# Kernel tuning notes

Measured on AMD Instinct MI355X. Metric: run time of the kernel, lower is better.

The kernel has to match this reference:

```python
import jax, jax.numpy as jnp
import numpy as np

HIDDEN_DIM = 4096
NUM_SHARDS = 64
TOP_K = 2
B = 16384


def setup_inputs() -> dict:
    key = jax.random.key(0)
    k_h, k_w = jax.random.split(key)
    h = jax.random.normal(k_h, (B, HIDDEN_DIM), dtype=jnp.float32)
    # nn.init.normal_(weight, std=0.02); bias zeros
    weight = jax.random.normal(k_w, (NUM_SHARDS, HIDDEN_DIM), dtype=jnp.float32) * 0.02
    bias = jnp.zeros((NUM_SHARDS,), dtype=jnp.float32)
    return {"h": h, "weight": weight, "bias": bias}


def reference(h, weight, bias):
    # logits: (B, num_shards)
    logits = jnp.einsum("bd,ed->be", h, weight) + bias
    probs = jax.nn.softmax(logits, axis=-1)
    k = min(TOP_K, weight.shape[0])
    topk_vals, topk_idx = jax.lax.top_k(probs, k)
    denom = jnp.maximum(jnp.sum(topk_vals, axis=-1, keepdims=True), 1e-12)
    topk_w = topk_vals / denom
    return topk_w, topk_idx
```

## Files before the change

kernel.cpp:

```cpp
#include <hip/hip_runtime.h>
#include <hip/hip_bf16.h>
#include <math.h>


#define HIDDEN 4096
#define NSHARD 64
#define B_ROWS 16384

typedef short bf16x8 __attribute__((ext_vector_type(8)));
typedef float f32x4  __attribute__((ext_vector_type(4)));

__device__ __forceinline__ unsigned short f32_to_bf16_rn(float f) {
    __hip_bfloat16 h = __float2bfloat16(f);
    return *reinterpret_cast<unsigned short*>(&h);
}
__device__ __forceinline__ float bf16_bits_to_f32(unsigned short u) {
    union { unsigned int i; float f; } v; v.i = ((unsigned int)u) << 16;
    return v.f;
}

__device__ __forceinline__ void bf16_split(float f, short* hi, short* lo) {
    const unsigned int u = __float_as_uint(f);
    const unsigned int r = u + 0x7fffu + ((u >> 16) & 1u);
    *hi = (short)(r >> 16);
    union { unsigned int i; float f2; } hv; hv.i = r & 0xffff0000u;
    const float res = f - hv.f2;
    const unsigned int u2 = __float_as_uint(res);
    *lo = (short)((u2 + 0x7fffu + ((u2 >> 16) & 1u)) >> 16);
}

__global__ __launch_bounds__(256)
void wsplit_kernel(const float* __restrict__ w,
                   unsigned short* __restrict__ w_hi,
                   unsigned short* __restrict__ w_lo)
{
    const int idx = (blockIdx.x * 256 + threadIdx.x) * 4;
    const float4 v = *(const float4*)(w + idx);
    const float a[4] = {v.x, v.y, v.z, v.w};
    ushort4 hi, lo;
    unsigned short hb;
    hb = f32_to_bf16_rn(a[0]); hi.x = hb; lo.x = f32_to_bf16_rn(a[0] - bf16_bits_to_f32(hb));
    hb = f32_to_bf16_rn(a[1]); hi.y = hb; lo.y = f32_to_bf16_rn(a[1] - bf16_bits_to_f32(hb));
    hb = f32_to_bf16_rn(a[2]); hi.z = hb; lo.z = f32_to_bf16_rn(a[2] - bf16_bits_to_f32(hb));
    hb = f32_to_bf16_rn(a[3]); hi.w = hb; lo.w = f32_to_bf16_rn(a[3] - bf16_bits_to_f32(hb));
    *(ushort4*)(w_hi + idx) = hi;
    *(ushort4*)(w_lo + idx) = lo;
}

__global__ __launch_bounds__(512, 8)
void gate_kernel(const float* __restrict__ h,
                 const unsigned short* __restrict__ w_hi,
                 const unsigned short* __restrict__ w_lo,
                 const float* __restrict__ bias,
                 float* __restrict__ out)
{
    __shared__ float lsum[4][16][68];

    const int tid  = threadIdx.x;
    const int lane = tid & 63;
    const int wv   = tid >> 6;
    const int q    = wv >> 1;
    const int jh   = wv & 1;
    const int m    = lane & 15;
    const int quad = lane >> 4;
    const int row0 = blockIdx.x * 16;

    const float* __restrict__ aptr =
        h + (size_t)(row0 + m) * HIDDEN + q * 1024 + quad * 8;
    const size_t boff = (size_t)m * HIDDEN + q * 1024 + quad * 8;
    const unsigned short* __restrict__ bh0p = w_hi + boff + (size_t)(jh * 2 + 0) * 16 * HIDDEN;
    const unsigned short* __restrict__ bh1p = w_hi + boff + (size_t)(jh * 2 + 1) * 16 * HIDDEN;
    const unsigned short* __restrict__ bl0p = w_lo + boff + (size_t)(jh * 2 + 0) * 16 * HIDDEN;
    const unsigned short* __restrict__ bl1p = w_lo + boff + (size_t)(jh * 2 + 1) * 16 * HIDDEN;

    f32x4 acch[2], accx[2];
#pragma unroll
    for (int j = 0; j < 2; ++j) {
        acch[j] = (f32x4)0.0f;
        accx[j] = (f32x4)0.0f;
    }

#pragma unroll
    for (int step = 0; step < 32; ++step) {
        const float4 a0 = *(const float4*)(aptr + step * 32);
        const float4 a1 = *(const float4*)(aptr + step * 32 + 4);
        const bf16x8 bh0 = *(const bf16x8*)(bh0p + step * 32);
        const bf16x8 bh1 = *(const bf16x8*)(bh1p + step * 32);
        const bf16x8 bl0 = *(const bf16x8*)(bl0p + step * 32);
        const bf16x8 bl1 = *(const bf16x8*)(bl1p + step * 32);

        const float av[8] = {a0.x, a0.y, a0.z, a0.w, a1.x, a1.y, a1.z, a1.w};
        bf16x8 ahi, alo;
#pragma unroll
        for (int i = 0; i < 8; ++i) {
            short hb, lb;
            bf16_split(av[i], &hb, &lb);
            ahi[i] = hb;
            alo[i] = lb;
        }

        acch[0] = __builtin_amdgcn_mfma_f32_16x16x32_bf16(ahi, bh0, acch[0], 0, 0, 0);
        acch[1] = __builtin_amdgcn_mfma_f32_16x16x32_bf16(ahi, bh1, acch[1], 0, 0, 0);
        accx[0] = __builtin_amdgcn_mfma_f32_16x16x32_bf16(alo, bh0, accx[0], 0, 0, 0);
        accx[1] = __builtin_amdgcn_mfma_f32_16x16x32_bf16(alo, bh1, accx[1], 0, 0, 0);
        accx[0] = __builtin_amdgcn_mfma_f32_16x16x32_bf16(ahi, bl0, accx[0], 0, 0, 0);
        accx[1] = __builtin_amdgcn_mfma_f32_16x16x32_bf16(ahi, bl1, accx[1], 0, 0, 0);
        accx[0] = __builtin_amdgcn_mfma_f32_16x16x32_bf16(alo, bl0, accx[0], 0, 0, 0);
        accx[1] = __builtin_amdgcn_mfma_f32_16x16x32_bf16(alo, bl1, accx[1], 0, 0, 0);
    }

#pragma unroll
    for (int j = 0; j < 2; ++j)
#pragma unroll
        for (int p = 0; p < 4; ++p)
            lsum[q][quad * 4 + p][(jh * 2 + j) * 16 + m] = acch[j][p] + accx[j][p];

    __syncthreads();

    if (tid < 256) {
        const int row = tid >> 4;
        const int s   = tid & 15;
        float4 vs = *(const float4*)&lsum[0][row][s * 4];
        {
            const float4 v1 = *(const float4*)&lsum[1][row][s * 4];
            const float4 v2 = *(const float4*)&lsum[2][row][s * 4];
            const float4 v3 = *(const float4*)&lsum[3][row][s * 4];
            vs.x += v1.x + v2.x + v3.x;
            vs.y += v1.y + v2.y + v3.y;
            vs.z += v1.z + v2.z + v3.z;
            vs.w += v1.w + v2.w + v3.w;
        }
        const float4 bv = *(const float4*)(bias + s * 4);
        const float v0 = vs.x + bv.x, v1 = vs.y + bv.y;
        const float v2 = vs.z + bv.z, v3 = vs.w + bv.w;

        float m1 = v0, m2 = -INFINITY;
        int   i1 = s * 4, i2 = 0;
        if (v1 > m1)      { m2 = m1; i2 = i1; m1 = v1; i1 = s * 4 + 1; }
        else              { m2 = v1; i2 = s * 4 + 1; }
        if (v2 > m1)      { m2 = m1; i2 = i1; m1 = v2; i1 = s * 4 + 2; }
        else if (v2 > m2) { m2 = v2; i2 = s * 4 + 2; }
        if (v3 > m1)      { m2 = m1; i2 = i1; m1 = v3; i1 = s * 4 + 3; }
        else if (v3 > m2) { m2 = v3; i2 = s * 4 + 3; }

#pragma unroll
        for (int msk = 1; msk <= 8; msk <<= 1) {
            const float o1 = __shfl_xor(m1, msk, 64);
            const int   q1 = __shfl_xor(i1, msk, 64);
            const float o2 = __shfl_xor(m2, msk, 64);
            const int   q2 = __shfl_xor(i2, msk, 64);
            const bool take = (o1 > m1) || (o1 == m1 && q1 < i1);
            const float w1 = take ? o1 : m1; const int w1i = take ? q1 : i1;
            const float l1 = take ? m1 : o1; const int l1i = take ? i1 : q1;
            const float s2 = take ? o2 : m2; const int s2i = take ? q2 : i2;
            const bool t2 = (l1 > s2) || (l1 == s2 && l1i < s2i);
            m1 = w1; i1 = w1i;
            m2 = t2 ? l1 : s2; i2 = t2 ? l1i : s2i;
        }

        if (s == 0) {
            const int orow = row0 + row;
            const float ed  = expf(m2 - m1);
            const float inv = 1.0f / (1.0f + ed);
            out[2 * orow + 0] = inv;
            out[2 * orow + 1] = ed * inv;
            float* __restrict__ oidx = out + 2 * B_ROWS;
            oidx[2 * orow + 0] = (float)i1;
            oidx[2 * orow + 1] = (float)i2;
        }
    }
}

extern "C" void kernel_launch(void* const* d_in, const int* in_sizes, int n_in,
                              void* d_out, int out_size, void* d_ws, size_t ws_size,
                              hipStream_t stream)
{
    const float* h    = (const float*)d_in[0];
    const float* wt   = (const float*)d_in[1];
    const float* bias = (const float*)d_in[2];
    float* out = (float*)d_out;

    unsigned short* w_hi = (unsigned short*)d_ws;
    unsigned short* w_lo = w_hi + (size_t)NSHARD * HIDDEN;

    wsplit_kernel<<<dim3(NSHARD * HIDDEN / 1024), dim3(256), 0, stream>>>(wt, w_hi, w_lo);
    gate_kernel<<<dim3(B_ROWS / 16), dim3(512), 0, stream>>>(h, w_hi, w_lo, bias, out);
}
```

Baseline: 485.5 us.

## Process 32 rows per block and double-buffer register loads in gate GEMM

Each block now handles two 16-row tiles, so every weight hi/lo fragment loaded from memory feeds twice as many MFMAs, halving weight traffic per row. The main loop also prefetches the next step's activation and weight fragments into a second register set while the current step computes. All 512 threads now run the top-2 reduction. Register use roughly doubles and the occupancy hint drops from 8 to 4, so there is less latency hiding from wave switching and only half as many blocks are launched.

```diff
diff --git a/kernel.cpp b/kernel.cpp
--- a/kernel.cpp
+++ b/kernel.cpp
@@ -47,14 +47,14 @@
     *(ushort4*)(w_lo + idx) = lo;
 }
 
-__global__ __launch_bounds__(512, 8)
+__global__ __launch_bounds__(512, 4)
 void gate_kernel(const float* __restrict__ h,
                  const unsigned short* __restrict__ w_hi,
                  const unsigned short* __restrict__ w_lo,
                  const float* __restrict__ bias,
                  float* __restrict__ out)
 {
-    __shared__ float lsum[4][16][68];
+    __shared__ float lsum[4][32][68];
 
     const int tid  = threadIdx.x;
     const int lane = tid & 63;
@@ -63,61 +63,88 @@
     const int jh   = wv & 1;
     const int m    = lane & 15;
     const int quad = lane >> 4;
-    const int row0 = blockIdx.x * 16;
-
-    const float* __restrict__ aptr =
+    const int row0 = blockIdx.x * 32;
+
+    const float* __restrict__ aptr0 =
         h + (size_t)(row0 + m) * HIDDEN + q * 1024 + quad * 8;
+    const float* __restrict__ aptr1 = aptr0 + (size_t)16 * HIDDEN;
     const size_t boff = (size_t)m * HIDDEN + q * 1024 + quad * 8;
     const unsigned short* __restrict__ bh0p = w_hi + boff + (size_t)(jh * 2 + 0) * 16 * HIDDEN;
     const unsigned short* __restrict__ bh1p = w_hi + boff + (size_t)(jh * 2 + 1) * 16 * HIDDEN;
     const unsigned short* __restrict__ bl0p = w_lo + boff + (size_t)(jh * 2 + 0) * 16 * HIDDEN;
     const unsigned short* __restrict__ bl1p = w_lo + boff + (size_t)(jh * 2 + 1) * 16 * HIDDEN;
 
-    f32x4 acch[2], accx[2];
-#pragma unroll
-    for (int j = 0; j < 2; ++j) {
-        acch[j] = (f32x4)0.0f;
-        accx[j] = (f32x4)0.0f;
+    f32x4 acch[2][2], accx[2][2];
+#pragma unroll
+    for (int rt = 0; rt < 2; ++rt)
+#pragma unroll
+        for (int j = 0; j < 2; ++j) {
+            acch[rt][j] = (f32x4)0.0f;
+            accx[rt][j] = (f32x4)0.0f;
+        }
+
+    float4 pa[2][2][2];
+    bf16x8 pbh[2][2], pbl[2][2];
+
+#define GATE_LOADS(S, T) do {                                              \
+        pa[S][0][0] = *(const float4*)(aptr0 + (T) * 32);                  \
+        pa[S][0][1] = *(const float4*)(aptr0 + (T) * 32 + 4);              \
+        pa[S][1][0] = *(const float4*)(aptr1 + (T) * 32);                  \
+        pa[S][1][1] = *(const float4*)(aptr1 + (T) * 32 + 4);              \
+        pbh[S][0]   = *(const bf16x8*)(bh0p + (T) * 32);                   \
+        pbh[S][1]   = *(const bf16x8*)(bh1p + (T) * 32);                   \
+        pbl[S][0]   = *(const bf16x8*)(bl0p + (T) * 32);                   \
+        pbl[S][1]   = *(const bf16x8*)(bl1p + (T) * 32);                   \
+    } while (0)
+
+    GATE_LOADS(0, 0);
+
+#pragma unroll
+    for (int step = 0; step < 32; ++step) {
+        const int cur = step & 1;
+        const int nxt = cur ^ 1;
+        if (step < 31) GATE_LOADS(nxt, step + 1);
+
+        bf16x8 ahi[2], alo[2];
+#pragma unroll
+        for (int rt = 0; rt < 2; ++rt) {
+            const float av[8] = {pa[cur][rt][0].x, pa[cur][rt][0].y,
+                                 pa[cur][rt][0].z, pa[cur][rt][0].w,
+                                 pa[cur][rt][1].x, pa[cur][rt][1].y,
+                                 pa[cur][rt][1].z, pa[cur][rt][1].w};
+#pragma unroll
+            for (int i = 0; i < 8; ++i) {
+                short hb, lb;
+                bf16_split(av[i], &hb, &lb);
+                ahi[rt][i] = hb;
+                alo[rt][i] = lb;
+            }
+        }
+
+#pragma unroll
+        for (int rt = 0; rt < 2; ++rt)
+#pragma unroll
+            for (int j = 0; j < 2; ++j) {
+                acch[rt][j] = __builtin_amdgcn_mfma_f32_16x16x32_bf16(ahi[rt], pbh[cur][j], acch[rt][j], 0, 0, 0);
+                accx[rt][j] = __builtin_amdgcn_mfma_f32_16x16x32_bf16(alo[rt], pbh[cur][j], accx[rt][j], 0, 0, 0);
+                accx[rt][j] = __builtin_amdgcn_mfma_f32_16x16x32_bf16(ahi[rt], pbl[cur][j], accx[rt][j], 0, 0, 0);
+                accx[rt][j] = __builtin_amdgcn_mfma_f32_16x16x32_bf16(alo[rt], pbl[cur][j], accx[rt][j], 0, 0, 0);
+            }
     }
-
-#pragma unroll
-    for (int step = 0; step < 32; ++step) {
-        const float4 a0 = *(const float4*)(aptr + step * 32);
-        const float4 a1 = *(const float4*)(aptr + step * 32 + 4);
-        const bf16x8 bh0 = *(const bf16x8*)(bh0p + step * 32);
-        const bf16x8 bh1 = *(const bf16x8*)(bh1p + step * 32);
-        const bf16x8 bl0 = *(const bf16x8*)(bl0p + step * 32);
-        const bf16x8 bl1 = *(const bf16x8*)(bl1p + step * 32);
-
-        const float av[8] = {a0.x, a0.y, a0.z, a0.w, a1.x, a1.y, a1.z, a1.w};
-        bf16x8 ahi, alo;
-#pragma unroll
-        for (int i = 0; i < 8; ++i) {
-            short hb, lb;
-            bf16_split(av[i], &hb, &lb);
-            ahi[i] = hb;
-            alo[i] = lb;
-        }
-
-        acch[0] = __builtin_amdgcn_mfma_f32_16x16x32_bf16(ahi, bh0, acch[0], 0, 0, 0);
-        acch[1] = __builtin_amdgcn_mfma_f32_16x16x32_bf16(ahi, bh1, acch[1], 0, 0, 0);
-        accx[0] = __builtin_amdgcn_mfma_f32_16x16x32_bf16(alo, bh0, accx[0], 0, 0, 0);
-        accx[1] = __builtin_amdgcn_mfma_f32_16x16x32_bf16(alo, bh1, accx[1], 0, 0, 0);
-        accx[0] = __builtin_amdgcn_mfma_f32_16x16x32_bf16(ahi, bl0, accx[0], 0, 0, 0);
-        accx[1] = __builtin_amdgcn_mfma_f32_16x16x32_bf16(ahi, bl1, accx[1], 0, 0, 0);
-        accx[0] = __builtin_amdgcn_mfma_f32_16x16x32_bf16(alo, bl0, accx[0], 0, 0, 0);
-        accx[1] = __builtin_amdgcn_mfma_f32_16x16x32_bf16(alo, bl1, accx[1], 0, 0, 0);
-    }
-
-#pragma unroll
-    for (int j = 0; j < 2; ++j)
-#pragma unroll
-        for (int p = 0; p < 4; ++p)
-            lsum[q][quad * 4 + p][(jh * 2 + j) * 16 + m] = acch[j][p] + accx[j][p];
+#undef GATE_LOADS
+
+#pragma unroll
+    for (int rt = 0; rt < 2; ++rt)
+#pragma unroll
+        for (int j = 0; j < 2; ++j)
+#pragma unroll
+            for (int p = 0; p < 4; ++p)
+                lsum[q][rt * 16 + quad * 4 + p][(jh * 2 + j) * 16 + m] =
+                    acch[rt][j][p] + accx[rt][j][p];
 
     __syncthreads();
 
-    if (tid < 256) {
+    {
         const int row = tid >> 4;
         const int s   = tid & 15;
         float4 vs = *(const float4*)&lsum[0][row][s * 4];
@@ -184,5 +211,5 @@
     unsigned short* w_lo = w_hi + (size_t)NSHARD * HIDDEN;
 
     wsplit_kernel<<<dim3(NSHARD * HIDDEN / 1024), dim3(256), 0, stream>>>(wt, w_hi, w_lo);
-    gate_kernel<<<dim3(B_ROWS / 16), dim3(512), 0, stream>>>(h, w_hi, w_lo, bias, out);
-}
+    gate_kernel<<<dim3(B_ROWS / 32), dim3(512), 0, stream>>>(h, w_hi, w_lo, bias, out);
+}
```

After: 428.1 us. 11.8% less time.
